# Optimization experiments

Measured on AMD Instinct MI355X. Metric: run time of the kernel, lower is better.

Reference implementation:

```python
import jax, jax.numpy as jnp
import numpy as np

EPSILON = 0.1
NSTEPS = 2
SIGN = 1.0  # forward integration (sample direction)


def setup_inputs() -> dict:
    key = jax.random.key(0)
    ks = jax.random.split(key, 6)
    B, D, H = 4096, 32, 256
    x = jax.random.normal(ks[0], (B, D), jnp.float32)
    logp = jax.random.normal(ks[1], (B,), jnp.float32)
    w1 = jax.random.normal(ks[2], (D, H), jnp.float32) / np.sqrt(D).astype(np.float32)
    b1 = jax.random.normal(ks[3], (H,), jnp.float32) * 0.01
    w2 = jax.random.normal(ks[4], (H,), jnp.float32) / np.sqrt(H).astype(np.float32)
    b2 = jax.random.normal(ks[5], (1,), jnp.float32) * 0.01
    return {"x": x, "logp": logp, "w1": w1, "b1": b1, "w2": w2, "b2": b2}


def reference(x, logp, w1, b1, w2, b2):
    D = x.shape[-1]

    def u(xi):  # scalar Brenier potential for a single sample [D] -> scalar
        h = jax.nn.softplus(xi @ w1 + b1)
        return h @ w2 + b2[0]

    grad_u = jax.grad(u)  # net.grad: du/dx, [D] -> [D]

    def lap_u(xi):  # net.laplacian: trace of Hessian via forward-over-reverse HVPs
        eye = jnp.eye(D, dtype=xi.dtype)
        hvp = lambda v: jax.jvp(grad_u, (xi,), (v,))[1]
        return jnp.trace(jax.vmap(hvp)(eye))

    v_grad = jax.vmap(grad_u)   # [B,D] -> [B,D]
    v_lap = jax.vmap(lap_u)     # [B,D] -> [B]

    def ode(xc):
        return SIGN * EPSILON * v_grad(xc), -SIGN * EPSILON * v_lap(xc)

    def step(carry, _):
        xc, lp = carry
        k1x, k1l = ode(xc)
        k2x, k2l = ode(xc + k1x / 2)
        k3x, k3l = ode(xc + k2x / 2)
        k4x, k4l = ode(xc + k3x)
        xc = xc + (k1x / 6.0 + k2x / 3.0 + k3x / 3.0 + k4x / 6.0)
        lp = lp + (k1l / 6.0 + k2l / 3.0 + k3l / 3.0 + k4l / 6.0)
        return (xc, lp), None

    (x, logp), _ = jax.lax.scan(step, (x, logp), None, length=NSTEPS)
    return x, logp
```

## Files before the change

kernel.cpp:

```cpp
#include <hip/hip_runtime.h>

#define B_TOTAL 4096
#define D 32
#define H 256
#define SPB 16
#define NW 8
#define HPW 32
#define ABS 20
#define PGS 36
#define XCS 40

static constexpr float EPS = 0.1f;

typedef __attribute__((ext_vector_type(8))) short short8v;
typedef __attribute__((ext_vector_type(4))) float f32x4;

__device__ __forceinline__ unsigned short bf16rne(float f) {
  unsigned u = __float_as_uint(f);
  u += 0x7FFFu + ((u >> 16) & 1u);
  return (unsigned short)(u >> 16);
}
__device__ __forceinline__ float fromb(unsigned short h) {
  return __uint_as_float(((unsigned)h) << 16);
}
__device__ __forceinline__ void split_rne(float f, unsigned short& hi, unsigned short& lo) {
  hi = bf16rne(f); lo = bf16rne(f - fromb(hi));
}

#define MFMA16(A, Bf, C) __builtin_amdgcn_mfma_f32_16x16x32_bf16((A), (Bf), (C), 0, 0, 0)


__global__ __launch_bounds__(512, 2) void ma_flow_kernel(
    const float* __restrict__ x_in, const float* __restrict__ logp_in,
    const float* __restrict__ w1, const float* __restrict__ b1,
    const float* __restrict__ w2, float* __restrict__ out)
{
  __shared__ __align__(16) unsigned aBuf[NW][SPB][ABS];
  __shared__ __align__(16) float partG[NW][SPB][PGS];
  __shared__ __align__(16) unsigned short xcH[SPB][XCS];
  __shared__ __align__(16) unsigned short xcL[SPB][XCS];

  const int tid = threadIdx.x;
  const int l  = tid & 63;
  const int wv = tid >> 6;
  const int lr = l & 15;
  const int lg = l >> 4;
  const int hbase = wv * HPW;
  const int s_own = tid >> 5;
  const int d_own = tid & 31;
  const int xci = ((d_own & 15) << 1) | (d_own >> 4);

  short8v Bzh[2], Bzl[2];
  float b1v[2], w2v[2], w2cv[2];
#pragma unroll
  for (int tau = 0; tau < 2; ++tau) {
    const int h = hbase + tau * 16 + lr;
    float cpart = 0.0f;
    short8v hi, lo;
#pragma unroll
    for (int j = 0; j < 8; ++j) {
      const int dj = lg * 4 + (j >> 1) + ((j & 1) << 4);
      float w = w1[dj * H + h];
      cpart = fmaf(w, w, cpart);
      unsigned short hb, lb; split_rne(w, hb, lb);
      hi[j] = (short)hb; lo[j] = (short)lb;
    }
    Bzh[tau] = hi; Bzl[tau] = lo;
    cpart += __shfl_xor(cpart, 16);
    cpart += __shfl_xor(cpart, 32);
    b1v[tau] = b1[h];
    float w2x = w2[h];
    w2v[tau] = w2x;
    w2cv[tau] = w2x * cpart;
  }
  short8v Bgh[2], Bgl[2];
#pragma unroll
  for (int nu = 0; nu < 2; ++nu) {
    const int d = nu * 16 + lr;
    short8v hi, lo;
#pragma unroll
    for (int j = 0; j < 8; ++j) {
      const int hl = lg * 4 + (j >> 1) + ((j & 1) << 4);
      float w = w1[d * H + hbase + hl];
      unsigned short hb, lb; split_rne(w, hb, lb);
      hi[j] = (short)hb; lo[j] = (short)lb;
    }
    Bgh[nu] = hi; Bgl[nu] = lo;
  }

  float x0r = x_in[blockIdx.x * (SPB * D) + tid];
  float accr = 0.0f;
  {
    unsigned u = __float_as_uint(x0r);
    xcH[s_own][xci] = (unsigned short)(u >> 16);
    float res = x0r - __uint_as_float(u & 0xFFFF0000u);
    xcL[s_own][xci] = (unsigned short)(__float_as_uint(res) >> 16);
  }
  float lp = (tid < SPB) ? logp_in[blockIdx.x * SPB + tid] : 0.0f;
  float lapAcc[4] = {0.0f, 0.0f, 0.0f, 0.0f};
  __syncthreads();

#pragma unroll 1
  for (int stage = 0; stage < 8; ++stage) {
    const int st = stage & 3;
    const float wa = (st == 0 || st == 3) ? (EPS / 6.0f) : (EPS / 3.0f);
    const float wc = (st == 2) ? EPS : (EPS * 0.5f);

    short8v ahi = *reinterpret_cast<const short8v*>(&xcH[lr][lg * 8]);
    short8v alo = *reinterpret_cast<const short8v*>(&xcL[lr][lg * 8]);

    f32x4 zz[2];
#pragma unroll
    for (int tau = 0; tau < 2; ++tau) {
      f32x4 z = {b1v[tau], b1v[tau], b1v[tau], b1v[tau]};
      z = MFMA16(ahi, Bzh[tau], z);
      z = MFMA16(alo, Bzh[tau], z);
      z = MFMA16(ahi, Bzl[tau], z);
      zz[tau] = z;
    }
#pragma unroll
    for (int r = 0; r < 4; ++r) {
      float E0 = __expf(-zz[0][r]);
      float t0 = __builtin_amdgcn_rcpf(1.0f + E0);
      float E1 = __expf(-zz[1][r]);
      float t1 = __builtin_amdgcn_rcpf(1.0f + E1);
      float q = fmaf(t1 * t1 * E1, w2cv[1], (t0 * t0 * E0) * w2cv[0]);
      lapAcc[r] = fmaf(wa, q, lapAcc[r]);
      aBuf[wv][lg * 4 + r][lr] =
          (unsigned)bf16rne(t0 * w2v[0]) | ((unsigned)bf16rne(t1 * w2v[1]) << 16);
    }

    asm volatile("s_waitcnt lgkmcnt(0)" ::: "memory");
    __builtin_amdgcn_sched_barrier(0);

    uint4 aq = *reinterpret_cast<const uint4*>(&aBuf[wv][lr][lg * 4]);
    short8v aF = *reinterpret_cast<const short8v*>(&aq);
#pragma unroll
    for (int nu = 0; nu < 2; ++nu) {
      f32x4 g = {0.0f, 0.0f, 0.0f, 0.0f};
      g = MFMA16(aF, Bgh[nu], g);
      g = MFMA16(aF, Bgl[nu], g);
#pragma unroll
      for (int r = 0; r < 4; ++r)
        partG[wv][lg * 4 + r][nu * 16 + lr] = g[r];
    }
    __syncthreads();

    float p0 = partG[0][s_own][d_own], p1 = partG[1][s_own][d_own];
    float p2 = partG[2][s_own][d_own], p3 = partG[3][s_own][d_own];
    float p4 = partG[4][s_own][d_own], p5 = partG[5][s_own][d_own];
    float p6 = partG[6][s_own][d_own], p7 = partG[7][s_own][d_own];
    float gsum = ((p0 + p1) + (p2 + p3)) + ((p4 + p5) + (p6 + p7));
    accr = fmaf(wa, gsum, accr);
    float xw;
    if (st < 3) {
      xw = fmaf(wc, gsum, x0r);
    } else {
      x0r += accr; accr = 0.0f; xw = x0r;
    }
    {
      unsigned u = __float_as_uint(xw);
      xcH[s_own][xci] = (unsigned short)(u >> 16);
      float res = xw - __uint_as_float(u & 0xFFFF0000u);
      xcL[s_own][xci] = (unsigned short)(__float_as_uint(res) >> 16);
    }
    __syncthreads();
  }

#pragma unroll
  for (int m = 1; m < 16; m <<= 1)
#pragma unroll
    for (int r = 0; r < 4; ++r) lapAcc[r] += __shfl_xor(lapAcc[r], m);
  if (lr == 0) {
#pragma unroll
    for (int r = 0; r < 4; ++r) partG[wv][lg * 4 + r][0] = lapAcc[r];
  }
  __syncthreads();

  out[blockIdx.x * (SPB * D) + tid] = x0r;
  if (tid < SPB) {
    float lt = 0.0f;
#pragma unroll
    for (int w = 0; w < NW; ++w) lt += partG[w][tid][0];
    out[B_TOTAL * D + blockIdx.x * SPB + tid] = lp - lt;
  }
}

extern "C" void kernel_launch(void* const* d_in, const int* in_sizes, int n_in,
                              void* d_out, int out_size, void* d_ws, size_t ws_size,
                              hipStream_t stream) {
  const float* x    = (const float*)d_in[0];
  const float* logp = (const float*)d_in[1];
  const float* w1   = (const float*)d_in[2];
  const float* b1   = (const float*)d_in[3];
  const float* w2   = (const float*)d_in[4];
  float* out = (float*)d_out;

  ma_flow_kernel<<<B_TOTAL / SPB, 512, 0, stream>>>(x, logp, w1, b1, w2, out);
}
```

Baseline: 15.26 us.

## Transpose first-layer MFMA to keep activations in registers, removing LDS round-trip

Swaps the MFMA operand order for the first layer so that each lane's output holds hidden units rather than samples. The output registers then directly form the A operand of the second-layer MFMA, so the activations no longer pass through an LDS buffer, a waitcnt or a sched barrier. Per-lane bias and weight vectors become f32x4 gathered via shuffles, and the w1 load layout for the second layer is reindexed to match. The laplacian reduction also simplifies to two shuffles, and the partG padding changes.

```diff
diff --git a/kernel.cpp b/kernel.cpp
--- a/kernel.cpp
+++ b/kernel.cpp
@@ -6,8 +6,7 @@
 #define SPB 16
 #define NW 8
 #define HPW 32
-#define ABS 20
-#define PGS 36
+#define PGS 34
 #define XCS 40
 
 static constexpr float EPS = 0.1f;
@@ -35,7 +34,6 @@
     const float* __restrict__ w1, const float* __restrict__ b1,
     const float* __restrict__ w2, float* __restrict__ out)
 {
-  __shared__ __align__(16) unsigned aBuf[NW][SPB][ABS];
   __shared__ __align__(16) float partG[NW][SPB][PGS];
   __shared__ __align__(16) unsigned short xcH[SPB][XCS];
   __shared__ __align__(16) unsigned short xcL[SPB][XCS];
@@ -51,7 +49,7 @@
   const int xci = ((d_own & 15) << 1) | (d_own >> 4);
 
   short8v Bzh[2], Bzl[2];
-  float b1v[2], w2v[2], w2cv[2];
+  float ctau[2];
 #pragma unroll
   for (int tau = 0; tau < 2; ++tau) {
     const int h = hbase + tau * 16 + lr;
@@ -68,11 +66,19 @@
     Bzh[tau] = hi; Bzl[tau] = lo;
     cpart += __shfl_xor(cpart, 16);
     cpart += __shfl_xor(cpart, 32);
-    b1v[tau] = b1[h];
-    float w2x = w2[h];
-    w2v[tau] = w2x;
-    w2cv[tau] = w2x * cpart;
+    ctau[tau] = cpart;
   }
+  f32x4 b1v[2], w2v[2], w2cv[2];
+#pragma unroll
+  for (int tau = 0; tau < 2; ++tau)
+#pragma unroll
+    for (int r = 0; r < 4; ++r) {
+      const int hh = hbase + tau * 16 + lg * 4 + r;
+      b1v[tau][r] = b1[hh];
+      float w2x = w2[hh];
+      w2v[tau][r] = w2x;
+      w2cv[tau][r] = w2x * __shfl(ctau[tau], lg * 4 + r);
+    }
   short8v Bgh[2], Bgl[2];
 #pragma unroll
   for (int nu = 0; nu < 2; ++nu) {
@@ -80,7 +86,7 @@
     short8v hi, lo;
 #pragma unroll
     for (int j = 0; j < 8; ++j) {
-      const int hl = lg * 4 + (j >> 1) + ((j & 1) << 4);
+      const int hl = ((j >> 2) << 4) + lg * 4 + (j & 3);
       float w = w1[d * H + hbase + hl];
       unsigned short hb, lb; split_rne(w, hb, lb);
       hi[j] = (short)hb; lo[j] = (short)lb;
@@ -97,7 +103,7 @@
     xcL[s_own][xci] = (unsigned short)(__float_as_uint(res) >> 16);
   }
   float lp = (tid < SPB) ? logp_in[blockIdx.x * SPB + tid] : 0.0f;
-  float lapAcc[4] = {0.0f, 0.0f, 0.0f, 0.0f};
+  float lapAcc = 0.0f;
   __syncthreads();
 
 #pragma unroll 1
@@ -106,35 +112,33 @@
     const float wa = (st == 0 || st == 3) ? (EPS / 6.0f) : (EPS / 3.0f);
     const float wc = (st == 2) ? EPS : (EPS * 0.5f);
 
-    short8v ahi = *reinterpret_cast<const short8v*>(&xcH[lr][lg * 8]);
-    short8v alo = *reinterpret_cast<const short8v*>(&xcL[lr][lg * 8]);
+    short8v xh = *reinterpret_cast<const short8v*>(&xcH[lr][lg * 8]);
+    short8v xl = *reinterpret_cast<const short8v*>(&xcL[lr][lg * 8]);
 
     f32x4 zz[2];
 #pragma unroll
     for (int tau = 0; tau < 2; ++tau) {
-      f32x4 z = {b1v[tau], b1v[tau], b1v[tau], b1v[tau]};
-      z = MFMA16(ahi, Bzh[tau], z);
-      z = MFMA16(alo, Bzh[tau], z);
-      z = MFMA16(ahi, Bzl[tau], z);
+      f32x4 z = MFMA16(Bzh[tau], xh, b1v[tau]);
+      z = MFMA16(Bzh[tau], xl, z);
+      z = MFMA16(Bzl[tau], xh, z);
       zz[tau] = z;
     }
+    float q = 0.0f;
+    unsigned short ab[2][4];
 #pragma unroll
-    for (int r = 0; r < 4; ++r) {
-      float E0 = __expf(-zz[0][r]);
-      float t0 = __builtin_amdgcn_rcpf(1.0f + E0);
-      float E1 = __expf(-zz[1][r]);
-      float t1 = __builtin_amdgcn_rcpf(1.0f + E1);
-      float q = fmaf(t1 * t1 * E1, w2cv[1], (t0 * t0 * E0) * w2cv[0]);
-      lapAcc[r] = fmaf(wa, q, lapAcc[r]);
-      aBuf[wv][lg * 4 + r][lr] =
-          (unsigned)bf16rne(t0 * w2v[0]) | ((unsigned)bf16rne(t1 * w2v[1]) << 16);
-    }
+    for (int tau = 0; tau < 2; ++tau)
+#pragma unroll
+      for (int r = 0; r < 4; ++r) {
+        float E = __expf(-zz[tau][r]);
+        float t = __builtin_amdgcn_rcpf(1.0f + E);
+        q = fmaf(t * t * E, w2cv[tau][r], q);
+        ab[tau][r] = bf16rne(t * w2v[tau][r]);
+      }
+    lapAcc = fmaf(wa, q, lapAcc);
+    short8v aF;
+#pragma unroll
+    for (int j = 0; j < 8; ++j) aF[j] = (short)ab[j >> 2][j & 3];
 
-    asm volatile("s_waitcnt lgkmcnt(0)" ::: "memory");
-    __builtin_amdgcn_sched_barrier(0);
-
-    uint4 aq = *reinterpret_cast<const uint4*>(&aBuf[wv][lr][lg * 4]);
-    short8v aF = *reinterpret_cast<const short8v*>(&aq);
 #pragma unroll
     for (int nu = 0; nu < 2; ++nu) {
       f32x4 g = {0.0f, 0.0f, 0.0f, 0.0f};
@@ -167,14 +171,9 @@
     __syncthreads();
   }
 
-#pragma unroll
-  for (int m = 1; m < 16; m <<= 1)
-#pragma unroll
-    for (int r = 0; r < 4; ++r) lapAcc[r] += __shfl_xor(lapAcc[r], m);
-  if (lr == 0) {
-#pragma unroll
-    for (int r = 0; r < 4; ++r) partG[wv][lg * 4 + r][0] = lapAcc[r];
-  }
+  lapAcc += __shfl_xor(lapAcc, 16);
+  lapAcc += __shfl_xor(lapAcc, 32);
+  if (l < 16) partG[wv][lr][0] = lapAcc;
   __syncthreads();
 
   out[blockIdx.x * (SPB * D) + tid] = x0r;
```

New measurement: 14.38 us. -5.8%, faster.
